# Performance work log

Measured on AMD Instinct MI355X. Metric: run time of the kernel, lower is better.

## Reference

```python
import jax, jax.numpy as jnp
import numpy as np

VOCAB, RANK, BEAM = 32000, 32, 64
B, S = 8, 512


def setup_inputs() -> dict:
    key = jax.random.key(0)
    k1, k2, k3, k4 = jax.random.split(key, 4)
    emissions = jax.random.normal(k1, (B, S, VOCAB), dtype=jnp.float32)
    targets = jax.random.randint(k2, (B, S), 0, VOCAB, dtype=jnp.int64)
    mask = jnp.ones((B, S), dtype=bool)
    E1 = jax.random.normal(k3, (VOCAB, RANK), dtype=jnp.float32) * 0.02
    E2 = jax.random.normal(k4, (VOCAB, RANK), dtype=jnp.float32) * 0.02
    return {"emissions": emissions, "targets": targets, "mask": mask, "E1": E1, "E2": E2}


def _compute_score(emissions, targets, mask, E1, E2):
    # gold emission scores: (B, S)
    em = jnp.take_along_axis(emissions, targets[:, :, None], axis=2)[:, :, 0]
    # low-rank transition scores between consecutive gold tokens: (B, S-1)
    trans = jnp.sum(E1[targets[:, :-1]] * E2[targets[:, 1:]], axis=-1)
    scores = em + jnp.pad(trans, ((0, 0), (1, 0)))
    scores = scores * mask.astype(scores.dtype)
    return scores.sum(-1)


def _compute_normalizer(emissions, targets, mask, E1, E2, beam=BEAM):
    b, s = targets.shape
    ib = jnp.arange(b)[:, None]
    it = jnp.arange(s)[None, :]
    # force the gold token into the beam by scattering +inf before top-k
    _em = emissions.at[ib, it, targets].set(jnp.inf)
    _, beam_targets = jax.lax.top_k(_em, beam)          # (B, S, beam)
    beam_em = jnp.take_along_axis(emissions, beam_targets, axis=2)  # (B, S, beam)
    # beam x beam transition matrices per step: (B, S-1, beam, beam)
    t1 = E1[beam_targets[:, :-1]]                        # (B, S-1, beam, rank)
    t2 = E2[beam_targets[:, 1:]]                         # (B, S-1, beam, rank)
    trans = jnp.einsum('bskr,bslr->bskl', t1, t2)

    def step(score, xs):
        tr, em, m = xs                                   # (B,beam,beam), (B,beam), (B,1)
        nxt = jax.nn.logsumexp(score[:, :, None] + tr, axis=1) + em
        return jnp.where(m, nxt, score), None

    xs = (jnp.swapaxes(trans, 0, 1),                     # (S-1, B, beam, beam)
          jnp.swapaxes(beam_em[:, 1:], 0, 1),            # (S-1, B, beam)
          jnp.swapaxes(mask[:, 1:, None], 0, 1))         # (S-1, B, 1)
    score, _ = jax.lax.scan(step, beam_em[:, 0], xs)
    return jax.nn.logsumexp(score, axis=1)


def reference(emissions, targets, mask, E1, E2):
    numerator = _compute_score(emissions, targets, mask, E1, E2)
    denominator = _compute_normalizer(emissions, targets, mask, E1, E2)
    llh = numerator - denominator
    return llh.sum(), llh
```

## Files before the change

kernel.cpp:

```cpp
#include <hip/hip_runtime.h>
#include <hip/hip_bf16.h>

#define VOCAB 32000
#define RANK  32
#define BEAM  64
#define BB    8
#define SS    512
#define KSEL  63
#define NPAIR 256

#define LOG2E 1.4426950408889634f
#define LN2   0.6931471805599453f

typedef _Float16 half2v __attribute__((ext_vector_type(2)));
typedef _Float16 half4  __attribute__((ext_vector_type(4)));
typedef _Float16 half8  __attribute__((ext_vector_type(8)));
typedef float    f32x4  __attribute__((ext_vector_type(4)));

__device__ __forceinline__ unsigned sortkey(float f) {
    unsigned u = __float_as_uint(f);
    return u ^ (((unsigned)((int)u >> 31)) | 0x80000000u);
}
__device__ __forceinline__ float keyfloat(unsigned k) {
    unsigned u = (k & 0x80000000u) ? (k ^ 0x80000000u) : ~k;
    return __uint_as_float(u);
}
__device__ __forceinline__ float wavesum(float x) {
    #pragma unroll
    for (int off = 32; off > 0; off >>= 1) x += __shfl_xor(x, off, 64);
    return x;
}
__device__ __forceinline__ float rl(float x, int lane) {
    return __builtin_bit_cast(float, __builtin_amdgcn_readlane(__builtin_bit_cast(int, x), lane));
}
__device__ __forceinline__ float rfl(float x) {
    return __builtin_bit_cast(float, __builtin_amdgcn_readfirstlane(__builtin_bit_cast(int, x)));
}
__device__ __forceinline__ float fdot2f(float a, float b, float c) {
#if __has_builtin(__builtin_amdgcn_fdot2)
    return __builtin_amdgcn_fdot2(__builtin_bit_cast(half2v, a),
                                  __builtin_bit_cast(half2v, b), c, false);
#else
    half2v ha = __builtin_bit_cast(half2v, a), hb = __builtin_bit_cast(half2v, b);
    return fmaf((float)ha.x, (float)hb.x, fmaf((float)ha.y, (float)hb.y, c));
#endif
}
__device__ __forceinline__ float dpp_xor1(float x) {
#if __has_builtin(__builtin_amdgcn_mov_dpp)
    return __builtin_bit_cast(float,
        __builtin_amdgcn_mov_dpp(__builtin_bit_cast(int, x), 0xB1, 0xF, 0xF, true));
#else
    return __shfl_xor(x, 1, 64);
#endif
}
__device__ __forceinline__ half8 loadrow_h8(const float* __restrict__ p) {
    half8 h;
    #pragma unroll
    for (int j = 0; j < 8; ++j) h[j] = (_Float16)p[j];
    return h;
}

__global__ __launch_bounds__(256) void num_kernel(
    const float* __restrict__ emissions, const int* __restrict__ targets,
    const float* __restrict__ E1, const float* __restrict__ E2,
    float* __restrict__ numer)
{
    int b = blockIdx.x, tid = threadIdx.x;
    float acc = 0.f;
    for (int s = tid; s < SS; s += 256) {
        int t = targets[b * SS + s];
        acc += emissions[((size_t)(b * SS + s)) * VOCAB + t];
        if (s > 0) {
            int tp = targets[b * SS + s - 1];
            const float* r1 = E1 + (size_t)tp * RANK;
            const float* r2 = E2 + (size_t)t * RANK;
            float d = 0.f;
            #pragma unroll
            for (int r = 0; r < RANK; ++r) d = fmaf(r1[r], r2[r], d);
            acc += d;
        }
    }
    __shared__ float red[256];
    red[tid] = acc;
    __syncthreads();
    for (int w = 128; w >= 1; w >>= 1) {
        if (tid < w) red[tid] += red[tid + w];
        __syncthreads();
    }
    if (tid == 0) numer[b] = red[0];
}

template<int NB>
__device__ __forceinline__ void select_from_hist(
    const unsigned* hist, unsigned need,
    unsigned* wsum , unsigned* result )
{
    constexpr int BPT = NB / 256;
    const int tid  = threadIdx.x;
    const int lane = tid & 63, wid = tid >> 6;
    const int base = tid * BPT;

    unsigned local = 0;
    #pragma unroll
    for (int i = 0; i < BPT; ++i) local += hist[base + i];

    unsigned x = local;
    #pragma unroll
    for (int off = 1; off < 64; off <<= 1) {
        unsigned v = __shfl_down(x, off, 64);
        x += (lane + off < 64) ? v : 0u;
    }
    if (lane == 0) wsum[wid] = x;
    __syncthreads();

    unsigned add = 0;
    #pragma unroll
    for (int w = 0; w < 4; ++w) add += (w > wid) ? wsum[w] : 0u;

    const unsigned S_incl = x + add;
    const unsigned S_excl = S_incl - local;
    if (S_excl < need && S_incl >= need) {
        unsigned cum = S_excl;
        #pragma unroll
        for (int i = BPT - 1; i >= 0; --i) {
            unsigned h = hist[base + i];
            if (cum + h >= need) { result[0] = (unsigned)(base + i); result[1] = need - cum; break; }
            cum += h;
        }
    }
    __syncthreads();
}

#define CCAP 512
__global__ __launch_bounds__(256) void topk_kernel(
    const float* __restrict__ emissions, const int* __restrict__ targets,
    int* __restrict__ beam_tgt, float* __restrict__ beam_em)
{
    __shared__ unsigned hist[2048];
    __shared__ unsigned s_ws[4];
    __shared__ unsigned s_sel[2];
    __shared__ unsigned s_cnt[2];
    __shared__ unsigned s_ccount;
    __shared__ unsigned ckey[CCAP];
    __shared__ unsigned cidx[CCAP];

    const int bs  = blockIdx.x;
    const int tid = threadIdx.x;
    const float* row = emissions + (size_t)bs * VOCAB;
    const int tgt = targets[bs];

    for (int i = tid; i < 2048; i += 256) hist[i] = 0;
    if (tid == 0) { s_ccount = 0; s_cnt[0] = 1; s_cnt[1] = 0; }
    __syncthreads();

    for (int i4 = tid; i4 < VOCAB / 4; i4 += 256) {
        float4 v = ((const float4*)row)[i4];
        int base = i4 * 4;
        #pragma unroll
        for (int j = 0; j < 4; ++j) {
            float f = (j == 0) ? v.x : (j == 1) ? v.y : (j == 2) ? v.z : v.w;
            int idx = base + j;
            if (idx != tgt) atomicAdd(&hist[sortkey(f) >> 21], 1u);
        }
    }
    __syncthreads();

    select_from_hist<2048>(hist, KSEL, s_ws, s_sel);
    const unsigned b1 = s_sel[0], need1 = s_sel[1];

    int*   bt = beam_tgt + (size_t)bs * BEAM;
    float* be = beam_em  + (size_t)bs * BEAM;

    for (int i4 = tid; i4 < VOCAB / 4; i4 += 256) {
        float4 v = ((const float4*)row)[i4];
        int base = i4 * 4;
        #pragma unroll
        for (int j = 0; j < 4; ++j) {
            float f = (j == 0) ? v.x : (j == 1) ? v.y : (j == 2) ? v.z : v.w;
            int idx = base + j;
            if (idx == tgt) continue;
            unsigned key = sortkey(f);
            unsigned bin = key >> 21;
            if (bin > b1) {
                unsigned p = atomicAdd(&s_cnt[0], 1u);
                if (p < BEAM) { bt[p] = idx; be[p] = f; }
            } else if (bin == b1) {
                unsigned c = atomicAdd(&s_ccount, 1u);
                if (c < CCAP) { ckey[c] = key; cidx[c] = idx; }
            }
        }
    }
    __syncthreads();
    const unsigned C = min(s_ccount, (unsigned)CCAP);

    for (int i = tid; i < 2048; i += 256) hist[i] = 0;
    __syncthreads();
    for (int i = tid; i < (int)C; i += 256) atomicAdd(&hist[(ckey[i] >> 10) & 2047], 1u);
    __syncthreads();
    select_from_hist<2048>(hist, need1, s_ws, s_sel);
    const unsigned b2 = s_sel[0], need2 = s_sel[1];

    for (int i = tid; i < 1024; i += 256) hist[i] = 0;
    __syncthreads();
    for (int i = tid; i < (int)C; i += 256) {
        unsigned k = ckey[i];
        if (((k >> 10) & 2047) == b2) atomicAdd(&hist[k & 1023], 1u);
    }
    __syncthreads();
    select_from_hist<1024>(hist, need2, s_ws, s_sel);
    const unsigned Kthr = (b1 << 21) | (b2 << 10) | s_sel[0];
    const unsigned tieNeed = s_sel[1];

    for (int i = tid; i < (int)C; i += 256) {
        unsigned k = ckey[i];
        if (k > Kthr) {
            unsigned p = atomicAdd(&s_cnt[0], 1u);
            if (p < BEAM) { bt[p] = cidx[i]; be[p] = keyfloat(k); }
        } else if (k == Kthr) {
            unsigned t = atomicAdd(&s_cnt[1], 1u);
            if (t < tieNeed) {
                unsigned p = atomicAdd(&s_cnt[0], 1u);
                if (p < BEAM) { bt[p] = cidx[i]; be[p] = keyfloat(k); }
            }
        }
    }
    if (tid == 0) { bt[0] = tgt; be[0] = row[tgt]; }
}

__global__ __launch_bounds__(256) void pair_kernel(
    const float* __restrict__ E1, const float* __restrict__ E2,
    const int* __restrict__ beam_tgt, const float* __restrict__ beam_em,
    unsigned short* __restrict__ Pbuf, float* __restrict__ scl)
{
    const int blk = blockIdx.x;
    const int b = blk >> 8, i = blk & 255;
    const int tid  = threadIdx.x;
    const int w    = tid >> 6;
    const int lane = tid & 63;
    const int hl   = lane & 15;
    const int kg   = lane >> 4;

    unsigned short* out = Pbuf + ((size_t)(b * NPAIR + i)) * (BEAM * BEAM);

    if (i == 255) {
        const int* btk = beam_tgt + ((size_t)(b * SS + 510)) * BEAM;
        const int* btl = btk + BEAM;
        const float* em = beam_em + ((size_t)(b * SS + 511)) * BEAM;

        half8 afrag = loadrow_h8(E2 + (size_t)btl[w * 16 + hl] * RANK + kg * 8);
        float emv[4];
        #pragma unroll
        for (int q = 0; q < 4; ++q) emv[q] = em[w * 16 + kg * 4 + q];

        #pragma unroll
        for (int t = 0; t < 4; ++t) {
            half8 bfrag = loadrow_h8(E1 + (size_t)btk[t * 16 + hl] * RANK + kg * 8);
            f32x4 acc = {0.f, 0.f, 0.f, 0.f};
            acc = __builtin_amdgcn_mfma_f32_16x16x32_f16(afrag, bfrag, acc, 0, 0, 0);
            #pragma unroll
            for (int q = 0; q < 4; ++q) {
                int lg  = w * 16 + kg * 4 + q;
                int kgc = t * 16 + hl;
                _Float16 h = (_Float16)exp2f((acc[q] + emv[q]) * LOG2E);
                out[(size_t)lg * BEAM + kgc] = __builtin_bit_cast(unsigned short, h);
            }
        }
        if (tid == 0) scl[(size_t)b * NPAIR + i] = 0.f;
        return;
    }

    const int* btA = beam_tgt + ((size_t)(b * SS + 2 * i)) * BEAM;
    const int* btB = btA + BEAM;
    const int* btC = btB + BEAM;
    const float* emB = beam_em + ((size_t)(b * SS + 2 * i + 1)) * BEAM;
    const float* emC = emB + BEAM;

    __shared__ _Float16 T1t[64][72];
    __shared__ _Float16 T2r[64][72];
    __shared__ float smax[4];

    half8 afrag1 = loadrow_h8(E2 + (size_t)btB[w * 16 + hl] * RANK + kg * 8);
    half8 afrag2 = loadrow_h8(E1 + (size_t)btB[w * 16 + hl] * RANK + kg * 8);
    float em1v[4];
    #pragma unroll
    for (int q = 0; q < 4; ++q) em1v[q] = emB[w * 16 + kg * 4 + q];

    #pragma unroll
    for (int t = 0; t < 4; ++t) {
        half8 bfrag = loadrow_h8(E1 + (size_t)btA[t * 16 + hl] * RANK + kg * 8);
        f32x4 acc = {0.f, 0.f, 0.f, 0.f};
        acc = __builtin_amdgcn_mfma_f32_16x16x32_f16(afrag1, bfrag, acc, 0, 0, 0);
        half4 hv;
        #pragma unroll
        for (int q = 0; q < 4; ++q) hv[q] = (_Float16)exp2f((acc[q] + em1v[q]) * LOG2E);
        *(half4*)&T1t[t * 16 + hl][w * 16 + kg * 4] = hv;
    }
    #pragma unroll
    for (int t = 0; t < 4; ++t) {
        half8 bfrag = loadrow_h8(E2 + (size_t)btC[t * 16 + hl] * RANK + kg * 8);
        float em2 = emC[t * 16 + hl];
        f32x4 acc = {0.f, 0.f, 0.f, 0.f};
        acc = __builtin_amdgcn_mfma_f32_16x16x32_f16(afrag2, bfrag, acc, 0, 0, 0);
        half4 hv;
        #pragma unroll
        for (int q = 0; q < 4; ++q) hv[q] = (_Float16)exp2f((acc[q] + em2) * LOG2E);
        *(half4*)&T2r[t * 16 + hl][w * 16 + kg * 4] = hv;
    }
    __syncthreads();

    const int ra = w * 16 + hl;
    half8 a0 = *(const half8*)&T1t[ra][kg * 8];
    half8 a1 = *(const half8*)&T1t[ra][32 + kg * 8];
    f32x4 pacc[4];
    float mp = -1e30f;
    #pragma unroll
    for (int t = 0; t < 4; ++t) {
        half8 c0 = *(const half8*)&T2r[t * 16 + hl][kg * 8];
        half8 c1 = *(const half8*)&T2r[t * 16 + hl][32 + kg * 8];
        f32x4 acc = {0.f, 0.f, 0.f, 0.f};
        acc = __builtin_amdgcn_mfma_f32_16x16x32_f16(a0, c0, acc, 0, 0, 0);
        acc = __builtin_amdgcn_mfma_f32_16x16x32_f16(a1, c1, acc, 0, 0, 0);
        pacc[t] = acc;
        #pragma unroll
        for (int q = 0; q < 4; ++q) mp = fmaxf(mp, acc[q]);
    }

    #pragma unroll
    for (int off = 32; off > 0; off >>= 1) mp = fmaxf(mp, __shfl_xor(mp, off, 64));
    if (lane == 0) smax[w] = mp;
    __syncthreads();
    float mx = fmaxf(fmaxf(smax[0], smax[1]), fmaxf(smax[2], smax[3]));
    float e  = ceilf(__log2f(mx));
    float c  = exp2f(-e);
    if (tid == 0) scl[(size_t)b * NPAIR + i] = e;

    #pragma unroll
    for (int t = 0; t < 4; ++t) {
        half4 hv;
        #pragma unroll
        for (int q = 0; q < 4; ++q) hv[q] = (_Float16)(pacc[t][q] * c);
        *(half4*)(out + (size_t)(t * 16 + hl) * BEAM + w * 16 + kg * 4) = hv;
    }
}

__global__ __launch_bounds__(64) void recur_kernel(
    const unsigned short* __restrict__ Pbuf, const float* __restrict__ beam_em,
    const float* __restrict__ scl, float* __restrict__ denom)
{
    int b = blockIdx.x, l = threadIdx.x;
    const float* bem = beam_em + (size_t)b * SS * BEAM;
    const float* scb = scl + (size_t)b * NPAIR;
    float sc = bem[l] * LOG2E;
    float M = rfl(sc);
    float v = exp2f(sc - M);

    const uint4* Trow = (const uint4*)(Pbuf + (size_t)b * NPAIR * (BEAM * BEAM)) + (size_t)l * 8;

    uint4 b0[8], b1[8], b2[8], b3[8];
    float l0, l1, l2, l3;

#define LOADT(BUF, STP) do { \
    const uint4* _p = Trow + (size_t)(STP) * 512; \
    _Pragma("unroll") \
    for (int i = 0; i < 8; ++i) BUF[i] = _p[i]; \
} while (0)

    LOADT(b0, 0); LOADT(b1, 1); LOADT(b2, 2); LOADT(b3, 3);
    l0 = scb[0]; l1 = scb[1]; l2 = scb[2]; l3 = scb[3];

#define STEP(BUF, LC) do { \
    float vn = dpp_xor1(v); \
    half2v ph; ph.x = (_Float16)v; ph.y = (_Float16)vn; \
    float pf = __builtin_bit_cast(float, ph);  \
    float a[8]; \
    _Pragma("unroll") \
    for (int i = 0; i < 8; ++i) { \
        uint4 t = BUF[i]; \
        float ai = fdot2f(rl(pf, 8 * i + 0), __builtin_bit_cast(float, t.x), 0.f); \
        ai = fdot2f(rl(pf, 8 * i + 2), __builtin_bit_cast(float, t.y), ai); \
        ai = fdot2f(rl(pf, 8 * i + 4), __builtin_bit_cast(float, t.z), ai); \
        ai = fdot2f(rl(pf, 8 * i + 6), __builtin_bit_cast(float, t.w), ai); \
        a[i] = ai; \
    } \
    float s = ((a[0] + a[1]) + (a[2] + a[3])) + ((a[4] + a[5]) + (a[6] + a[7])); \
    float v0 = rfl(s); \
    M += __log2f(v0) + (LC);            \
    v = s * __builtin_amdgcn_rcpf(v0); \
} while (0)

    for (int t = 0; t < 252; t += 4) {
        STEP(b0, l0); LOADT(b0, t + 4); l0 = scb[t + 4];
        STEP(b1, l1); LOADT(b1, t + 5); l1 = scb[t + 5];
        STEP(b2, l2); LOADT(b2, t + 6); l2 = scb[t + 6];
        STEP(b3, l3); LOADT(b3, t + 7); l3 = scb[t + 7];
    }
    STEP(b0, l0);
    STEP(b1, l1);
    STEP(b2, l2);
    STEP(b3, l3);

    float s = wavesum(v);
    if (l == 0) denom[b] = (__log2f(s) + M) * LN2;
#undef STEP
#undef LOADT
}

__global__ __launch_bounds__(64) void fin_kernel(
    const float* __restrict__ numer, const float* __restrict__ denom,
    float* __restrict__ out)
{
    int tid = threadIdx.x;
    float llh = 0.f;
    if (tid < BB) {
        llh = numer[tid] - denom[tid];
        out[1 + tid] = llh;
    }
    float s = llh;
    #pragma unroll
    for (int off = 4; off > 0; off >>= 1) s += __shfl_xor(s, off, 64);
    if (tid == 0) out[0] = s;
}

extern "C" void kernel_launch(void* const* d_in, const int* in_sizes, int n_in,
                              void* d_out, int out_size, void* d_ws, size_t ws_size,
                              hipStream_t stream) {
    const float* emissions = (const float*)d_in[0];
    const int*   targets   = (const int*)d_in[1];
    const float* E1        = (const float*)d_in[3];
    const float* E2        = (const float*)d_in[4];
    float* out = (float*)d_out;

    char* w = (char*)d_ws;
    float* numer = (float*)w;
    float* denom = (float*)(w + 256);
    float* scl   = (float*)(w + 1024);
    int*   btgt  = (int*)(w + 16384);
    float* bem   = (float*)(w + 16384 + (1u << 20));
    unsigned short* Pbuf = (unsigned short*)(w + 16384 + (2u << 20));

    num_kernel  <<<BB, 256, 0, stream>>>(emissions, targets, E1, E2, numer);
    topk_kernel <<<BB * SS, 256, 0, stream>>>(emissions, targets, btgt, bem);
    pair_kernel <<<BB * NPAIR, 256, 0, stream>>>(E1, E2, btgt, bem, Pbuf, scl);
    recur_kernel<<<BB, 64, 0, stream>>>(Pbuf, bem, scl, denom);
    fin_kernel  <<<1, 64, 0, stream>>>(numer, denom, out);
}
```

Before: 851.3 us.

## Fold pair transition matrices into octets and stash top bins in topk

Adds a fold kernel that multiplies consecutive pair matrices with MFMA (pairs into quads, quads into octets), so the serial recurrence runs 64 steps per batch instead of 256. Each fold renormalizes by a power of two and accumulates the log scales. The top-k kernel now builds the histogram and stashes high-bin candidates in one pass over the row, skipping the second full read of the row when the stash suffices. The cost is two extra launches, extra fp16 rounding from the repeated matrix products, and more shared memory in top-k.

```diff
diff --git a/kernel.cpp b/kernel.cpp
--- a/kernel.cpp
+++ b/kernel.cpp
@@ -8,6 +8,8 @@
 #define SS    512
 #define KSEL  63
 #define NPAIR 256
+#define NQUAD 128
+#define NOCT  64
 
 #define LOG2E 1.4426950408889634f
 #define LN2   0.6931471805599453f
@@ -132,6 +134,8 @@
 }
 
 #define CCAP 512
+#define SCAP 512
+#define STASH_BIN 1537u
 __global__ __launch_bounds__(256) void topk_kernel(
     const float* __restrict__ emissions, const int* __restrict__ targets,
     int* __restrict__ beam_tgt, float* __restrict__ beam_em)
@@ -141,6 +145,9 @@
     __shared__ unsigned s_sel[2];
     __shared__ unsigned s_cnt[2];
     __shared__ unsigned s_ccount;
+    __shared__ unsigned s_scount;
+    __shared__ unsigned skey[SCAP];
+    __shared__ unsigned sidx[SCAP];
     __shared__ unsigned ckey[CCAP];
     __shared__ unsigned cidx[CCAP];
 
@@ -150,26 +157,8 @@
     const int tgt = targets[bs];
 
     for (int i = tid; i < 2048; i += 256) hist[i] = 0;
-    if (tid == 0) { s_ccount = 0; s_cnt[0] = 1; s_cnt[1] = 0; }
-    __syncthreads();
-
-    for (int i4 = tid; i4 < VOCAB / 4; i4 += 256) {
-        float4 v = ((const float4*)row)[i4];
-        int base = i4 * 4;
-        #pragma unroll
-        for (int j = 0; j < 4; ++j) {
-            float f = (j == 0) ? v.x : (j == 1) ? v.y : (j == 2) ? v.z : v.w;
-            int idx = base + j;
-            if (idx != tgt) atomicAdd(&hist[sortkey(f) >> 21], 1u);
-        }
-    }
-    __syncthreads();
-
-    select_from_hist<2048>(hist, KSEL, s_ws, s_sel);
-    const unsigned b1 = s_sel[0], need1 = s_sel[1];
-
-    int*   bt = beam_tgt + (size_t)bs * BEAM;
-    float* be = beam_em  + (size_t)bs * BEAM;
+    if (tid == 0) { s_ccount = 0; s_scount = 0; s_cnt[0] = 1; s_cnt[1] = 0; }
+    __syncthreads();
 
     for (int i4 = tid; i4 < VOCAB / 4; i4 += 256) {
         float4 v = ((const float4*)row)[i4];
@@ -181,12 +170,53 @@
             if (idx == tgt) continue;
             unsigned key = sortkey(f);
             unsigned bin = key >> 21;
+            atomicAdd(&hist[bin], 1u);
+            if (bin >= STASH_BIN) {
+                unsigned c = atomicAdd(&s_scount, 1u);
+                if (c < SCAP) { skey[c] = key; sidx[c] = idx; }
+            }
+        }
+    }
+    __syncthreads();
+
+    select_from_hist<2048>(hist, KSEL, s_ws, s_sel);
+    const unsigned b1 = s_sel[0], need1 = s_sel[1];
+
+    int*   bt = beam_tgt + (size_t)bs * BEAM;
+    float* be = beam_em  + (size_t)bs * BEAM;
+
+    const bool fast = (b1 >= STASH_BIN) && (s_scount <= SCAP);
+
+    if (fast) {
+        const unsigned S = s_scount;
+        for (int i = tid; i < (int)S; i += 256) {
+            unsigned k = skey[i], bin = k >> 21;
             if (bin > b1) {
                 unsigned p = atomicAdd(&s_cnt[0], 1u);
-                if (p < BEAM) { bt[p] = idx; be[p] = f; }
+                if (p < BEAM) { bt[p] = sidx[i]; be[p] = keyfloat(k); }
             } else if (bin == b1) {
                 unsigned c = atomicAdd(&s_ccount, 1u);
-                if (c < CCAP) { ckey[c] = key; cidx[c] = idx; }
+                ckey[c] = k; cidx[c] = sidx[i];
+            }
+        }
+    } else {
+        for (int i4 = tid; i4 < VOCAB / 4; i4 += 256) {
+            float4 v = ((const float4*)row)[i4];
+            int base = i4 * 4;
+            #pragma unroll
+            for (int j = 0; j < 4; ++j) {
+                float f = (j == 0) ? v.x : (j == 1) ? v.y : (j == 2) ? v.z : v.w;
+                int idx = base + j;
+                if (idx == tgt) continue;
+                unsigned key = sortkey(f);
+                unsigned bin = key >> 21;
+                if (bin > b1) {
+                    unsigned p = atomicAdd(&s_cnt[0], 1u);
+                    if (p < BEAM) { bt[p] = idx; be[p] = f; }
+                } else if (bin == b1) {
+                    unsigned c = atomicAdd(&s_ccount, 1u);
+                    if (c < CCAP) { ckey[c] = key; cidx[c] = idx; }
+                }
             }
         }
     }
@@ -343,18 +373,92 @@
     }
 }
 
+template<int NIN>
+__global__ __launch_bounds__(256) void fold_kernel(
+    const unsigned short* __restrict__ Pin, const float* __restrict__ sin_,
+    unsigned short* __restrict__ Pout, float* __restrict__ sout)
+{
+    constexpr int NOUT = NIN / 2;
+    const int blk = blockIdx.x;
+    const int b = blk / NOUT, j = blk % NOUT;
+    const int tid  = threadIdx.x;
+    const int w    = tid >> 6;
+    const int lane = tid & 63;
+    const int hl   = lane & 15;
+    const int kg   = lane >> 4;
+
+    __shared__ _Float16 At[64][72];
+    __shared__ _Float16 Br[64][72];
+    __shared__ float smax[4];
+
+    const unsigned short* A = Pin + ((size_t)(b * NIN + 2 * j)) * (BEAM * BEAM);
+    const unsigned short* B = A + BEAM * BEAM;
+
+    {
+        int r = tid >> 2, c = (tid & 3) * 16;
+        half8 vb0 = *(const half8*)(B + r * BEAM + c);
+        half8 vb1 = *(const half8*)(B + r * BEAM + c + 8);
+        *(half8*)&Br[r][c]     = vb0;
+        *(half8*)&Br[r][c + 8] = vb1;
+        half8 va0 = *(const half8*)(A + r * BEAM + c);
+        half8 va1 = *(const half8*)(A + r * BEAM + c + 8);
+        #pragma unroll
+        for (int q = 0; q < 8; ++q) At[c + q][r]     = va0[q];
+        #pragma unroll
+        for (int q = 0; q < 8; ++q) At[c + 8 + q][r] = va1[q];
+    }
+    __syncthreads();
+
+    const int ra = w * 16 + hl;
+    half8 a0 = *(const half8*)&At[ra][kg * 8];
+    half8 a1 = *(const half8*)&At[ra][32 + kg * 8];
+    f32x4 pacc[4];
+    float mp = -1e30f;
+    #pragma unroll
+    for (int t = 0; t < 4; ++t) {
+        half8 c0 = *(const half8*)&Br[t * 16 + hl][kg * 8];
+        half8 c1 = *(const half8*)&Br[t * 16 + hl][32 + kg * 8];
+        f32x4 acc = {0.f, 0.f, 0.f, 0.f};
+        acc = __builtin_amdgcn_mfma_f32_16x16x32_f16(a0, c0, acc, 0, 0, 0);
+        acc = __builtin_amdgcn_mfma_f32_16x16x32_f16(a1, c1, acc, 0, 0, 0);
+        pacc[t] = acc;
+        #pragma unroll
+        for (int q = 0; q < 4; ++q) mp = fmaxf(mp, acc[q]);
+    }
+
+    #pragma unroll
+    for (int off = 32; off > 0; off >>= 1) mp = fmaxf(mp, __shfl_xor(mp, off, 64));
+    if (lane == 0) smax[w] = mp;
+    __syncthreads();
+    float mx = fmaxf(fmaxf(smax[0], smax[1]), fmaxf(smax[2], smax[3]));
+    float e  = ceilf(__log2f(mx));
+    float c  = exp2f(-e);
+    if (tid == 0)
+        sout[(size_t)b * NOUT + j] = sin_[(size_t)b * NIN + 2 * j]
+                                   + sin_[(size_t)b * NIN + 2 * j + 1] + e;
+
+    unsigned short* out = Pout + ((size_t)(b * NOUT + j)) * (BEAM * BEAM);
+    #pragma unroll
+    for (int t = 0; t < 4; ++t) {
+        half4 hv;
+        #pragma unroll
+        for (int q = 0; q < 4; ++q) hv[q] = (_Float16)(pacc[t][q] * c);
+        *(half4*)(out + (size_t)(t * 16 + hl) * BEAM + w * 16 + kg * 4) = hv;
+    }
+}
+
 __global__ __launch_bounds__(64) void recur_kernel(
-    const unsigned short* __restrict__ Pbuf, const float* __restrict__ beam_em,
+    const unsigned short* __restrict__ Obuf, const float* __restrict__ beam_em,
     const float* __restrict__ scl, float* __restrict__ denom)
 {
     int b = blockIdx.x, l = threadIdx.x;
     const float* bem = beam_em + (size_t)b * SS * BEAM;
-    const float* scb = scl + (size_t)b * NPAIR;
+    const float* scb = scl + (size_t)b * NOCT;
     float sc = bem[l] * LOG2E;
     float M = rfl(sc);
     float v = exp2f(sc - M);
 
-    const uint4* Trow = (const uint4*)(Pbuf + (size_t)b * NPAIR * (BEAM * BEAM)) + (size_t)l * 8;
+    const uint4* Trow = (const uint4*)(Obuf + (size_t)b * NOCT * (BEAM * BEAM)) + (size_t)l * 8;
 
     uint4 b0[8], b1[8], b2[8], b3[8];
     float l0, l1, l2, l3;
@@ -388,7 +492,7 @@
     v = s * __builtin_amdgcn_rcpf(v0); \
 } while (0)
 
-    for (int t = 0; t < 252; t += 4) {
+    for (int t = 0; t < 60; t += 4) {
         STEP(b0, l0); LOADT(b0, t + 4); l0 = scb[t + 4];
         STEP(b1, l1); LOADT(b1, t + 5); l1 = scb[t + 5];
         STEP(b2, l2); LOADT(b2, t + 6); l2 = scb[t + 6];
@@ -433,14 +537,20 @@
     char* w = (char*)d_ws;
     float* numer = (float*)w;
     float* denom = (float*)(w + 256);
-    float* scl   = (float*)(w + 1024);
-    int*   btgt  = (int*)(w + 16384);
-    float* bem   = (float*)(w + 16384 + (1u << 20));
-    unsigned short* Pbuf = (unsigned short*)(w + 16384 + (2u << 20));
-
-    num_kernel  <<<BB, 256, 0, stream>>>(emissions, targets, E1, E2, numer);
-    topk_kernel <<<BB * SS, 256, 0, stream>>>(emissions, targets, btgt, bem);
-    pair_kernel <<<BB * NPAIR, 256, 0, stream>>>(E1, E2, btgt, bem, Pbuf, scl);
-    recur_kernel<<<BB, 64, 0, stream>>>(Pbuf, bem, scl, denom);
-    fin_kernel  <<<1, 64, 0, stream>>>(numer, denom, out);
-}
+    float* sclP  = (float*)(w + 4096);
+    float* sclQ  = (float*)(w + 16384);
+    float* sclO  = (float*)(w + 24576);
+    int*   btgt  = (int*)(w + 65536);
+    float* bem   = (float*)(w + 65536 + (1u << 20));
+    unsigned short* Pbuf = (unsigned short*)(w + 65536 + (2u  << 20));
+    unsigned short* Qbuf = (unsigned short*)(w + 65536 + (18u << 20));
+    unsigned short* Obuf = (unsigned short*)(w + 65536 + (26u << 20));
+
+    num_kernel        <<<BB, 256, 0, stream>>>(emissions, targets, E1, E2, numer);
+    topk_kernel       <<<BB * SS, 256, 0, stream>>>(emissions, targets, btgt, bem);
+    pair_kernel       <<<BB * NPAIR, 256, 0, stream>>>(E1, E2, btgt, bem, Pbuf, sclP);
+    fold_kernel<NPAIR><<<BB * NQUAD, 256, 0, stream>>>(Pbuf, sclP, Qbuf, sclQ);
+    fold_kernel<NQUAD><<<BB * NOCT,  256, 0, stream>>>(Qbuf, sclQ, Obuf, sclO);
+    recur_kernel      <<<BB, 64, 0, stream>>>(Obuf, bem, sclO, denom);
+    fin_kernel        <<<1, 64, 0, stream>>>(numer, denom, out);
+}
```

Measured after the change: 747.8 us. 12.2% less time.
